# Kernel optimization log

Measured on AMD Instinct MI355X. Metric: run time of the kernel, lower is better.

The kernel has to match this reference:

```python
import jax, jax.numpy as jnp
import numpy as np

B, T, D = 8, 1024, 768
H, DH = 12, 64
E, K, DFF = 16, 2, 3072
EPS = 1e-5


def _ln(x, w, b):
    m = x.mean(-1, keepdims=True)
    v = ((x - m) ** 2).mean(-1, keepdims=True)
    return (x - m) * jax.lax.rsqrt(v + EPS) * w + b


def setup_inputs() -> dict:
    key = jax.random.key(0)
    ks = jax.random.split(key, 12)
    s = 0.02
    return {
        "x": jax.random.normal(ks[0], (B, T, D), jnp.float32),
        "ln1_w": jnp.ones((D,), jnp.float32),
        "ln1_b": jnp.zeros((D,), jnp.float32),
        "qkv_w": jax.random.normal(ks[1], (D, 3 * D), jnp.float32) * s,
        "qkv_b": jnp.zeros((3 * D,), jnp.float32),
        "proj_w": jax.random.normal(ks[2], (D, D), jnp.float32) * s,
        "proj_b": jnp.zeros((D,), jnp.float32),
        "ln2_w": jnp.ones((D,), jnp.float32),
        "ln2_b": jnp.zeros((D,), jnp.float32),
        "router_w": jax.random.normal(ks[3], (D, E), jnp.float32) * s,
        "w1": jax.random.normal(ks[4], (E, D, DFF), jnp.float32) * s,
        "b1": jnp.zeros((E, DFF), jnp.float32),
        "w2": jax.random.normal(ks[5], (E, DFF, D), jnp.float32) * s,
        "b2": jnp.zeros((E, D), jnp.float32),
    }


def _block(x, ln1_w, ln1_b, qkv_w, qkv_b, proj_w, proj_b,
           ln2_w, ln2_b, router_w, w1, b1, w2, b2):
    # --- attention ---
    h = _ln(x, ln1_w, ln1_b)
    qkv = h @ qkv_w + qkv_b                      # [B,T,3D]
    q, k, v = jnp.split(qkv, 3, axis=-1)
    q = q.reshape(B, T, H, DH).transpose(0, 2, 1, 3)
    k = k.reshape(B, T, H, DH).transpose(0, 2, 1, 3)
    v = v.reshape(B, T, H, DH).transpose(0, 2, 1, 3)
    scores = jnp.einsum("bhqd,bhkd->bhqk", q, k) / np.sqrt(DH)
    causal = jnp.tril(jnp.ones((T, T), bool))
    scores = jnp.where(causal, scores, -jnp.inf)
    attn = jax.nn.softmax(scores, axis=-1)
    y = jnp.einsum("bhqk,bhkd->bhqd", attn, v)
    y = y.transpose(0, 2, 1, 3).reshape(B, T, D)
    x = x + y @ proj_w + proj_b                  # residual 1

    # --- MoE FFN (dense all-experts, gated combine) ---
    z = _ln(x, ln2_w, ln2_b)                     # [B,T,D]
    probs = jax.nn.softmax(z @ router_w, axis=-1)  # [B,T,E]
    top_p, ix = jax.lax.top_k(probs, K)
    gate = (jax.nn.one_hot(ix, E, dtype=probs.dtype) * top_p[..., None]).sum(-2)  # [B,T,E]
    gate_e = jnp.moveaxis(gate, -1, 0)           # [E,B,T]

    def body(acc, ew):
        g, W1, B1, W2, B2 = ew
        out = jax.nn.gelu(z @ W1 + B1, approximate=False) @ W2 + B2
        return acc + g[..., None] * out, None

    yff, _ = jax.lax.scan(body, jnp.zeros_like(z), (gate_e, w1, b1, w2, b2))
    # MoELayer returns z + yff; Block adds x again (faithful double residual)
    return x + z + yff


def reference(x, ln1_w, ln1_b, qkv_w, qkv_b, proj_w, proj_b,
              ln2_w, ln2_b, router_w, w1, b1, w2, b2):
    return _block(x, ln1_w, ln1_b, qkv_w, qkv_b, proj_w, proj_b,
                  ln2_w, ln2_b, router_w, w1, b1, w2, b2)
```

## Files before the change

### kernel.cpp

```cpp
#include <hip/hip_runtime.h>
#include <math.h>

#define D_MODEL 768
#define T_SEQ   1024
#define B_BATCH 8
#define NTOK    8192
#define H_HEADS 12
#define DHEAD   64
#define NEXP    16
#define DFF     3072
#define NPAIR   16384
#define MAXT128 144
#define MAXT256 80

typedef unsigned short u16;
typedef unsigned int   u32;

typedef __attribute__((ext_vector_type(8))) short bf16x8;
typedef __attribute__((ext_vector_type(4))) float f32x4;
typedef __attribute__((ext_vector_type(4))) u32   u32x4;

__device__ __forceinline__ float bf2f(u16 u) { return __uint_as_float(((u32)u) << 16); }
__device__ __forceinline__ u16 f2bf(float f) {
    u32 u = __float_as_uint(f);
    return (u16)((u + 0x7FFFu + ((u >> 16) & 1u)) >> 16);
}

__device__ __forceinline__ float fast_gelu(float v) {
    float u2 = -1.5957691216f * v * (1.0f + 0.044715f * v * v);
    return v / (1.0f + __expf(u2));
}

__device__ __forceinline__ void gload16(const void* g, void* l) {
    __builtin_amdgcn_global_load_lds((const __attribute__((address_space(1))) void*)g,
                                     (__attribute__((address_space(3))) void*)l, 16, 0, 0);
}

__global__ __launch_bounds__(256) void ln_kernel(const float* __restrict__ x,
                                                 const float* __restrict__ w,
                                                 const float* __restrict__ b,
                                                 u16* __restrict__ out_bf,
                                                 float* __restrict__ out_f) {
    const int row = blockIdx.x;
    const int tid = threadIdx.x;
    const float* xr = x + (size_t)row * D_MODEL;
    float v0 = xr[tid], v1 = xr[tid + 256], v2 = xr[tid + 512];
    float s = v0 + v1 + v2;
    float s2 = v0 * v0 + v1 * v1 + v2 * v2;
#pragma unroll
    for (int o = 32; o > 0; o >>= 1) { s += __shfl_down(s, o); s2 += __shfl_down(s2, o); }
    __shared__ float red[8];
    __shared__ float stats[2];
    const int wid = tid >> 6;
    if ((tid & 63) == 0) { red[wid] = s; red[4 + wid] = s2; }
    __syncthreads();
    if (tid == 0) {
        float ts = red[0] + red[1] + red[2] + red[3];
        float ts2 = red[4] + red[5] + red[6] + red[7];
        float mean = ts * (1.0f / D_MODEL);
        float var = ts2 * (1.0f / D_MODEL) - mean * mean;
        stats[0] = mean;
        stats[1] = rsqrtf(var + 1e-5f);
    }
    __syncthreads();
    const float mean = stats[0], rstd = stats[1];
    u16* orow = out_bf + (size_t)row * D_MODEL;
    float r0 = (v0 - mean) * rstd * w[tid]       + b[tid];
    float r1 = (v1 - mean) * rstd * w[tid + 256] + b[tid + 256];
    float r2 = (v2 - mean) * rstd * w[tid + 512] + b[tid + 512];
    orow[tid] = f2bf(r0); orow[tid + 256] = f2bf(r1); orow[tid + 512] = f2bf(r2);
    if (out_f) {
        float* frow = out_f + (size_t)row * D_MODEL;
        frow[tid] = r0; frow[tid + 256] = r1; frow[tid + 512] = r2;
    }
}

__global__ __launch_bounds__(256) void transpose_cvt(const float* __restrict__ src,
                                                     u16* __restrict__ dst,
                                                     int R, int C) {
    const size_t plane = (size_t)R * C;
    src += (size_t)blockIdx.z * plane;
    dst += (size_t)blockIdx.z * plane;
    __shared__ __align__(16) u16 tile[64][72];
    const int t = threadIdx.x;
    const int r0 = blockIdx.y * 64, c0 = blockIdx.x * 64;
    {
        const int lr = t >> 2, lc = (t & 3) * 16;
        const float* sp = src + (size_t)(r0 + lr) * C + c0 + lc;
        u16 tmp[16];
#pragma unroll
        for (int j = 0; j < 4; ++j) {
            f32x4 f = *(const f32x4*)(sp + j * 4);
            tmp[j * 4 + 0] = f2bf(f[0]); tmp[j * 4 + 1] = f2bf(f[1]);
            tmp[j * 4 + 2] = f2bf(f[2]); tmp[j * 4 + 3] = f2bf(f[3]);
        }
        *(u32x4*)&tile[lr][lc]     = *(const u32x4*)&tmp[0];
        *(u32x4*)&tile[lr][lc + 8] = *(const u32x4*)&tmp[8];
    }
    __syncthreads();
    {
        const int ln = t >> 2, lk0 = (t & 3) * 16;
        u16 o[16];
#pragma unroll
        for (int j = 0; j < 16; ++j) o[j] = tile[lk0 + j][ln];
        u16* d = dst + (size_t)(c0 + ln) * R + r0 + lk0;
        *(u32x4*)&d[0] = *(const u32x4*)&o[0];
        *(u32x4*)&d[8] = *(const u32x4*)&o[8];
    }
}

template <int MODE>
__global__ __launch_bounds__(512, 4) void gemm256(
    const u16* __restrict__ A, const u16* __restrict__ Bt,
    const float* __restrict__ bias, void* __restrict__ Cout,
    const float* __restrict__ resid,
    const int* __restrict__ bucket_tok, const int* __restrict__ offsets,
    const int* __restrict__ counts, const int* __restrict__ desc_e,
    const int* __restrict__ desc_r, const int* __restrict__ tile_cnt,
    int K, int N)
{
    const u32 nwg  = gridDim.x * gridDim.y;
    const u32 orig = blockIdx.x + gridDim.x * blockIdx.y;
    const u32 flat = (nwg & 7u) ? orig : ((orig & 7u) * (nwg >> 3) + (orig >> 3));
    const int bx = (int)(flat % gridDim.x);
    const int by = (int)(flat / gridDim.x);

    int e = 0, r0 = 0, off = 0, ne = 0, row0 = 0;
    const int col0 = bx * 128;
    if constexpr (MODE >= 2) {
        if (by >= *tile_cnt) return;
        e = desc_e[by];
        r0 = desc_r[by];
        off = offsets[e];
        ne = counts[e];
    } else {
        row0 = by * 256;
    }
    if constexpr (MODE == 2) Bt += (size_t)e * D_MODEL * DFF;
    if constexpr (MODE == 3) Bt += (size_t)e * DFF * D_MODEL;

    __shared__ __align__(16) u16 AsBs[256 * 64 + 128 * 64];
    u16* As = AsBs;
    u16* Bs = AsBs + 256 * 64;

    const int tid = threadIdx.x;
    const int lane = tid & 63;
    const int w = tid >> 6;
    const int wm = w >> 1, wn = w & 1;
    const int fr = lane & 15, fg = lane >> 4;

    const int koff = ((((tid & 7) * 16) ^ (((tid >> 3) & 7) << 4)) >> 1);

    u32 aoff[4];
#pragma unroll
    for (int i = 0; i < 4; ++i) {
        const int r = i * 64 + (tid >> 3);
        u32 row;
        if constexpr (MODE == 2) {
            int rb = r0 + r;
            row = (u32)bucket_tok[off + (rb < ne ? rb : 0)];
        } else if constexpr (MODE == 3) {
            int rb = r0 + r;
            row = (u32)(off + (rb < ne ? rb : (ne - 1)));
        } else {
            row = (u32)(row0 + r);
        }
        aoff[i] = row * (u32)K + (u32)koff;
    }
    u32 boff[2];
#pragma unroll
    for (int i = 0; i < 2; ++i) {
        const int n = i * 64 + (tid >> 3);
        boff[i] = (u32)(col0 + n) * (u32)K + (u32)koff;
    }

    f32x4 acc[4][4] = {};

    for (int k0 = 0; k0 < K; k0 += 64) {
        __syncthreads();
#pragma unroll
        for (int i = 0; i < 4; ++i)
            gload16(A + aoff[i] + k0, &As[(i * 512 + w * 64) * 8]);
#pragma unroll
        for (int i = 0; i < 2; ++i)
            gload16(Bt + boff[i] + k0, &Bs[(i * 512 + w * 64) * 8]);
        __syncthreads();
#pragma unroll
        for (int kk = 0; kk < 2; ++kk) {
            const int sw = ((kk * 64 + fg * 16) ^ ((fr & 7) << 4)) >> 1;
            bf16x8 a[4], b[4];
#pragma unroll
            for (int mi = 0; mi < 4; ++mi)
                a[mi] = *(const bf16x8*)&As[(wm * 64 + mi * 16 + fr) * 64 + sw];
#pragma unroll
            for (int ni = 0; ni < 4; ++ni)
                b[ni] = *(const bf16x8*)&Bs[(wn * 64 + ni * 16 + fr) * 64 + sw];
#pragma unroll
            for (int mi = 0; mi < 4; ++mi)
#pragma unroll
                for (int ni = 0; ni < 4; ++ni)
                    acc[mi][ni] = __builtin_amdgcn_mfma_f32_16x16x32_bf16(a[mi], b[ni], acc[mi][ni], 0, 0, 0);
        }
    }

    __syncthreads();
    float* slab = (float*)AsBs + w * 1088;
    const int er = lane >> 2;
    const int ec = (lane & 3) * 16;
    const int colb = col0 + wn * 64 + ec;

#pragma unroll
    for (int mi = 0; mi < 4; ++mi) {
#pragma unroll
        for (int ni = 0; ni < 4; ++ni)
#pragma unroll
            for (int i = 0; i < 4; ++i)
                slab[(fg * 4 + i) * 68 + ni * 16 + fr] = acc[mi][ni][i];
        __syncthreads();
        f32x4 v[4];
#pragma unroll
        for (int q = 0; q < 4; ++q) v[q] = *(const f32x4*)&slab[er * 68 + ec + q * 4];
        const int lrow = wm * 64 + mi * 16 + er;

        if constexpr (MODE == 0) {
            u16 o[16];
#pragma unroll
            for (int q = 0; q < 4; ++q) {
                f32x4 b4 = *(const f32x4*)&bias[colb + q * 4];
#pragma unroll
                for (int j = 0; j < 4; ++j) o[q * 4 + j] = f2bf(v[q][j] + b4[j]);
            }
            u16* cp = (u16*)Cout + (size_t)(row0 + lrow) * N + colb;
            *(u32x4*)cp       = *(const u32x4*)&o[0];
            *(u32x4*)(cp + 8) = *(const u32x4*)&o[8];
        } else if constexpr (MODE == 1) {
            float* cp = (float*)Cout + (size_t)(row0 + lrow) * N + colb;
            const float* rp = resid + (size_t)(row0 + lrow) * N + colb;
#pragma unroll
            for (int q = 0; q < 4; ++q) {
                f32x4 b4 = *(const f32x4*)&bias[colb + q * 4];
                f32x4 r4 = *(const f32x4*)(rp + q * 4);
                f32x4 o4;
#pragma unroll
                for (int j = 0; j < 4; ++j) o4[j] = v[q][j] + b4[j] + r4[j];
                *(f32x4*)(cp + q * 4) = o4;
            }
        } else if constexpr (MODE == 2) {
            const int rb = r0 + lrow;
            if (rb < ne) {
                u16 o[16];
#pragma unroll
                for (int q = 0; q < 4; ++q) {
                    f32x4 b4 = *(const f32x4*)&bias[(size_t)e * DFF + colb + q * 4];
#pragma unroll
                    for (int j = 0; j < 4; ++j) o[q * 4 + j] = f2bf(fast_gelu(v[q][j] + b4[j]));
                }
                u16* cp = (u16*)Cout + (size_t)(off + rb) * N + colb;
                *(u32x4*)cp       = *(const u32x4*)&o[0];
                *(u32x4*)(cp + 8) = *(const u32x4*)&o[8];
            }
        } else {
            const int rb = r0 + lrow;
            if (rb < ne) {
                float* cp = (float*)Cout + (size_t)(off + rb) * N + colb;
#pragma unroll
                for (int q = 0; q < 4; ++q) {
                    f32x4 b4 = *(const f32x4*)&bias[(size_t)e * D_MODEL + colb + q * 4];
                    f32x4 o4;
#pragma unroll
                    for (int j = 0; j < 4; ++j) o4[j] = v[q][j] + b4[j];
                    *(f32x4*)(cp + q * 4) = o4;
                }
            }
        }
        if (mi < 3) __syncthreads();
    }
}

template <int MODE>
__global__ __launch_bounds__(256) void gemm128f(
    const u16* __restrict__ A, const float* __restrict__ Bf,
    const float* __restrict__ bias, void* __restrict__ Cout,
    const float* __restrict__ resid,
    const int* __restrict__ bucket_tok, const int* __restrict__ offsets,
    const int* __restrict__ counts, const int* __restrict__ desc_e,
    const int* __restrict__ desc_r, const int* __restrict__ tile_cnt,
    int K, int N)
{
    int e = 0, r0 = 0, off = 0, ne = 0, row0 = 0;
    const int col0 = blockIdx.x * 128;
    if constexpr (MODE >= 2) {
        if ((int)blockIdx.y >= *tile_cnt) return;
        e = desc_e[blockIdx.y]; r0 = desc_r[blockIdx.y];
        off = offsets[e]; ne = counts[e];
    } else row0 = blockIdx.y * 128;
    if constexpr (MODE == 2) Bf += (size_t)e * D_MODEL * DFF;
    if constexpr (MODE == 3) Bf += (size_t)e * DFF * D_MODEL;

    __shared__ __align__(16) u16 AsL[128 * 32];
    __shared__ __align__(16) u16 BsL[128 * 32];

    const int tid = threadIdx.x;
    const int lane = tid & 63;
    const int w = tid >> 6;
    const int wr = (w >> 1) * 64, wc = (w & 1) * 64;
    const int fr = lane & 15, fg = lane >> 4;
    const int lrow = lane >> 2, lk = (lane & 3) * 8;

    const u16* ag[2];
#pragma unroll
    for (int i = 0; i < 2; ++i) {
        int r = i * 64 + w * 16 + lrow;
        size_t srow;
        if constexpr (MODE == 2) {
            int rb = r0 + r;
            int tok = bucket_tok[off + (rb < ne ? rb : 0)];
            srow = (size_t)tok * K;
        } else if constexpr (MODE == 3) {
            int rb = r0 + r;
            int pp = off + (rb < ne ? rb : (ne - 1));
            srow = (size_t)pp * K;
        } else srow = (size_t)(row0 + r) * K;
        ag[i] = A + srow + lk;
    }

    f32x4 acc[4][4] = {};
    for (int k0 = 0; k0 < K; k0 += 32) {
        __syncthreads();
        gload16(ag[0] + k0, &AsL[0 * 2048 + w * 512]);
        gload16(ag[1] + k0, &AsL[1 * 2048 + w * 512]);
#pragma unroll
        for (int i = 0; i < 4; ++i) {
            int s = tid + 256 * i;
            int kk = s >> 5, n4 = (s & 31) * 4;
            f32x4 f = *(const f32x4*)(Bf + (size_t)(k0 + kk) * N + col0 + n4);
            BsL[(n4 + 0) * 32 + kk] = f2bf(f[0]);
            BsL[(n4 + 1) * 32 + kk] = f2bf(f[1]);
            BsL[(n4 + 2) * 32 + kk] = f2bf(f[2]);
            BsL[(n4 + 3) * 32 + kk] = f2bf(f[3]);
        }
        __syncthreads();
        bf16x8 a[4], b[4];
#pragma unroll
        for (int mi = 0; mi < 4; ++mi)
            a[mi] = *(const bf16x8*)&AsL[(wr + mi * 16 + fr) * 32 + fg * 8];
#pragma unroll
        for (int ni = 0; ni < 4; ++ni)
            b[ni] = *(const bf16x8*)&BsL[(wc + ni * 16 + fr) * 32 + fg * 8];
#pragma unroll
        for (int mi = 0; mi < 4; ++mi)
#pragma unroll
            for (int ni = 0; ni < 4; ++ni)
                acc[mi][ni] = __builtin_amdgcn_mfma_f32_16x16x32_bf16(a[mi], b[ni], acc[mi][ni], 0, 0, 0);
    }
#pragma unroll
    for (int mi = 0; mi < 4; ++mi) {
#pragma unroll
        for (int ni = 0; ni < 4; ++ni) {
            const int lr = wr + mi * 16 + fg * 4;
            const int col = col0 + wc + ni * 16 + fr;
#pragma unroll
            for (int i = 0; i < 4; ++i) {
                float v = acc[mi][ni][i];
                if constexpr (MODE == 0) {
                    int grow = row0 + lr + i;
                    ((u16*)Cout)[(size_t)grow * N + col] = f2bf(v + bias[col]);
                } else if constexpr (MODE == 1) {
                    int grow = row0 + lr + i;
                    size_t idx = (size_t)grow * N + col;
                    ((float*)Cout)[idx] = resid[idx] + v + bias[col];
                } else if constexpr (MODE == 2) {
                    int rb = r0 + lr + i;
                    if (rb < ne) {
                        float vb = v + bias[(size_t)e * DFF + col];
                        ((u16*)Cout)[(size_t)(off + rb) * N + col] = f2bf(fast_gelu(vb));
                    }
                } else {
                    int rb = r0 + lr + i;
                    if (rb < ne) {
                        ((float*)Cout)[(size_t)(off + rb) * N + col] = v + bias[(size_t)e * D_MODEL + col];
                    }
                }
            }
        }
    }
}

__global__ __launch_bounds__(256) void attn_mfma(const u16* __restrict__ qkv,
                                                 u16* __restrict__ y) {
    const int bh = blockIdx.x;
    const int b = bh / H_HEADS, h = bh % H_HEADS;
    const int qt = gridDim.y - 1 - blockIdx.y;
    const int tid = threadIdx.x, lane = tid & 63, w = tid >> 6;
    const int fr = lane & 15, fg = lane >> 4;

    __shared__ __align__(16) u16 Ks[64][72];
    __shared__ __align__(16) u16 Vt[64][72];
    __shared__ __align__(16) u16 Ps[4][32][72];

    const int tb = b * T_SEQ + qt * 128;
    const int wrow = w * 32;

    bf16x8 aq[2][2];
#pragma unroll
    for (int rg = 0; rg < 2; ++rg) {
        const u16* qp = qkv + (size_t)(tb + wrow + rg * 16 + fr) * (3 * D_MODEL) + h * DHEAD + fg * 8;
        aq[rg][0] = *(const bf16x8*)qp;
        aq[rg][1] = *(const bf16x8*)(qp + 32);
    }
    f32x4 accO[2][4] = {};
    float m_[2][4], l_[2][4];
#pragma unroll
    for (int rg = 0; rg < 2; ++rg)
#pragma unroll
        for (int i = 0; i < 4; ++i) { m_[rg][i] = -1e30f; l_[rg][i] = 0.0f; }

    const int ktmax = 2 * qt + 1;
    for (int kt = 0; kt <= ktmax; ++kt) {
        __syncthreads();
        {
            const int krow = tid >> 2, c16 = (tid & 3) * 16;
            const u16* kp = qkv + (size_t)(b * T_SEQ + kt * 64 + krow) * (3 * D_MODEL)
                          + D_MODEL + h * DHEAD + c16;
            *(u32x4*)&Ks[krow][c16]     = *(const u32x4*)kp;
            *(u32x4*)&Ks[krow][c16 + 8] = *(const u32x4*)(kp + 8);
            const u16* vp = kp + D_MODEL;
            u16 vv[16];
            *(u32x4*)&vv[0] = *(const u32x4*)vp;
            *(u32x4*)&vv[8] = *(const u32x4*)(vp + 8);
#pragma unroll
            for (int j = 0; j < 16; ++j) Vt[c16 + j][krow] = vv[j];
        }
        __syncthreads();

        if (kt * 64 > qt * 128 + wrow + 31) continue;

#pragma unroll
        for (int rg = 0; rg < 2; ++rg) {
            f32x4 s4[4] = {};
#pragma unroll
            for (int kk = 0; kk < 2; ++kk) {
#pragma unroll
                for (int ni = 0; ni < 4; ++ni) {
                    bf16x8 bk = *(const bf16x8*)&Ks[ni * 16 + fr][kk * 32 + fg * 8];
                    s4[ni] = __builtin_amdgcn_mfma_f32_16x16x32_bf16(aq[rg][kk], bk, s4[ni], 0, 0, 0);
                }
            }
            float p[4][4];
#pragma unroll
            for (int i = 0; i < 4; ++i) {
                const int grow = qt * 128 + wrow + rg * 16 + fg * 4 + i;
                float rmax = -1e30f;
#pragma unroll
                for (int ni = 0; ni < 4; ++ni) {
                    float v = s4[ni][i] * 0.125f;
                    if (kt * 64 + ni * 16 + fr > grow) v = -1e30f;
                    p[ni][i] = v;
                    rmax = fmaxf(rmax, v);
                }
#pragma unroll
                for (int msk = 1; msk < 16; msk <<= 1) rmax = fmaxf(rmax, __shfl_xor(rmax, msk));
                const float mn = fmaxf(m_[rg][i], rmax);
                float sum = 0.0f;
#pragma unroll
                for (int ni = 0; ni < 4; ++ni) {
                    float ev = __expf(p[ni][i] - mn);
                    p[ni][i] = ev;
                    sum += ev;
                }
#pragma unroll
                for (int msk = 1; msk < 16; msk <<= 1) sum += __shfl_xor(sum, msk);
                const float sc = __expf(m_[rg][i] - mn);
                l_[rg][i] = l_[rg][i] * sc + sum;
                m_[rg][i] = mn;
#pragma unroll
                for (int ni = 0; ni < 4; ++ni) accO[rg][ni][i] *= sc;
#pragma unroll
                for (int ni = 0; ni < 4; ++ni)
                    Ps[w][rg * 16 + fg * 4 + i][ni * 16 + fr] = f2bf(p[ni][i]);
            }
        }

#pragma unroll
        for (int rg = 0; rg < 2; ++rg) {
#pragma unroll
            for (int kk = 0; kk < 2; ++kk) {
                bf16x8 ap = *(const bf16x8*)&Ps[w][rg * 16 + fr][kk * 32 + fg * 8];
#pragma unroll
                for (int ni = 0; ni < 4; ++ni) {
                    bf16x8 bv = *(const bf16x8*)&Vt[ni * 16 + fr][kk * 32 + fg * 8];
                    accO[rg][ni] = __builtin_amdgcn_mfma_f32_16x16x32_bf16(ap, bv, accO[rg][ni], 0, 0, 0);
                }
            }
        }
    }

#pragma unroll
    for (int rg = 0; rg < 2; ++rg) {
#pragma unroll
        for (int i = 0; i < 4; ++i) {
            const float inv = 1.0f / l_[rg][i];
            u16* yp = y + (size_t)(tb + wrow + rg * 16 + fg * 4 + i) * D_MODEL + h * DHEAD;
#pragma unroll
            for (int ni = 0; ni < 4; ++ni) yp[ni * 16 + fr] = f2bf(accO[rg][ni][i] * inv);
        }
    }
}

__global__ __launch_bounds__(64) void router_kernel(const float* __restrict__ z,
                                                    const float* __restrict__ rw,
                                                    float* __restrict__ gates,
                                                    int* __restrict__ eidx) {
    const int t = blockIdx.x;
    const int lane = threadIdx.x;
    const int e = lane & 15, part = lane >> 4;
    const float* zr = z + (size_t)t * D_MODEL;
    float acc = 0.0f;
    for (int d = part * 192; d < part * 192 + 192; ++d)
        acc += zr[d] * rw[d * NEXP + e];
    acc += __shfl_down(acc, 32);
    acc += __shfl_down(acc, 16);
    const float lg = acc;
    float logit[NEXP];
#pragma unroll
    for (int ee = 0; ee < NEXP; ++ee) logit[ee] = __shfl(lg, ee);
    if (lane == 0) {
        float m1 = -1e30f, m2 = -1e30f; int i1 = 0, i2 = 0;
#pragma unroll
        for (int ee = 0; ee < NEXP; ++ee) {
            float v = logit[ee];
            if (v > m1) { m2 = m1; i2 = i1; m1 = v; i1 = ee; }
            else if (v > m2) { m2 = v; i2 = ee; }
        }
        float den = 0.0f;
#pragma unroll
        for (int ee = 0; ee < NEXP; ++ee) den += __expf(logit[ee] - m1);
        const float inv = 1.0f / den;
        gates[2 * t] = inv;
        gates[2 * t + 1] = __expf(m2 - m1) * inv;
        eidx[2 * t] = i1;
        eidx[2 * t + 1] = i2;
    }
}

__global__ __launch_bounds__(256) void count_kernel(const int* __restrict__ eidx, int* counts) {
    int i = blockIdx.x * 256 + threadIdx.x;
    if (i < NPAIR) atomicAdd(&counts[eidx[i]], 1);
}

__global__ void offsets_kernel(const int* __restrict__ counts, int* offsets, int* cursor,
                               int* desc_e, int* desc_r, int* tile_cnt, int step) {
    if (threadIdx.x == 0 && blockIdx.x == 0) {
        int off = 0, nt = 0;
        for (int e = 0; e < NEXP; ++e) {
            offsets[e] = off;
            cursor[e] = off;
            int c = counts[e];
            for (int r = 0; r < c; r += step) { desc_e[nt] = e; desc_r[nt] = r; ++nt; }
            off += c;
        }
        *tile_cnt = nt;
    }
}

__global__ __launch_bounds__(256) void scatter_kernel(const int* __restrict__ eidx, int* cursor,
                                                      int* __restrict__ btok, int* __restrict__ ppos) {
    int i = blockIdx.x * 256 + threadIdx.x;
    if (i < NPAIR) {
        int pos = atomicAdd(&cursor[eidx[i]], 1);
        btok[pos] = i >> 1;
        ppos[i] = pos;
    }
}

__global__ __launch_bounds__(256) void final_kernel(const float* __restrict__ x1,
                                                    const float* __restrict__ zf,
                                                    const float* __restrict__ moe_o,
                                                    const float* __restrict__ gates,
                                                    const int* __restrict__ ppos,
                                                    float* __restrict__ out) {
    const int t = blockIdx.x;
    const int d = blockIdx.y * 256 + threadIdx.x;
    const size_t idx = (size_t)t * D_MODEL + d;
    const float g0 = gates[2 * t], g1 = gates[2 * t + 1];
    const int p0 = ppos[2 * t], p1 = ppos[2 * t + 1];
    out[idx] = x1[idx] + zf[idx] + g0 * moe_o[(size_t)p0 * D_MODEL + d]
                                 + g1 * moe_o[(size_t)p1 * D_MODEL + d];
}

extern "C" void kernel_launch(void* const* d_in, const int* in_sizes, int n_in,
                              void* d_out, int out_size, void* d_ws, size_t ws_size,
                              hipStream_t stream) {
    const float* x        = (const float*)d_in[0];
    const float* ln1_w    = (const float*)d_in[1];
    const float* ln1_b    = (const float*)d_in[2];
    const float* qkv_w    = (const float*)d_in[3];
    const float* qkv_b    = (const float*)d_in[4];
    const float* proj_w   = (const float*)d_in[5];
    const float* proj_b   = (const float*)d_in[6];
    const float* ln2_w    = (const float*)d_in[7];
    const float* ln2_b    = (const float*)d_in[8];
    const float* router_w = (const float*)d_in[9];
    const float* w1       = (const float*)d_in[10];
    const float* b1       = (const float*)d_in[11];
    const float* w2       = (const float*)d_in[12];
    const float* b2       = (const float*)d_in[13];
    float* out = (float*)d_out;

    char* ws = (char*)d_ws;
    size_t off = 0;
    auto alloc = [&](size_t bytes) -> void* {
        void* p = ws + off;
        off += (bytes + 255) & ~(size_t)255;
        return p;
    };
    u16*  h_bf   = (u16*)alloc((size_t)NTOK * D_MODEL * 2);
    u16*  qkv_bf = (u16*)alloc((size_t)NTOK * 3 * D_MODEL * 2);
    u16*  y_bf   = h_bf;
    float* x1    = (float*)alloc((size_t)NTOK * D_MODEL * 4);
    u16*  z_bf   = (u16*)alloc((size_t)NTOK * D_MODEL * 2);
    float* z_f   = (float*)alloc((size_t)NTOK * D_MODEL * 4);
    u16*  act    = (u16*)alloc((size_t)NPAIR * DFF * 2);
    float* moe_o = (float*)alloc((size_t)NPAIR * D_MODEL * 4);
    float* gates = (float*)alloc((size_t)NTOK * 2 * 4);
    int*  eidx   = (int*)alloc((size_t)NTOK * 2 * 4);
    int*  ppos   = (int*)alloc((size_t)NTOK * 2 * 4);
    int*  btok   = (int*)alloc((size_t)NPAIR * 4);
    int*  counts = (int*)alloc(NEXP * 4);
    int*  offs   = (int*)alloc(NEXP * 4);
    int*  cursor = (int*)alloc(NEXP * 4);
    int*  desc_e = (int*)alloc(MAXT128 * 4);
    int*  desc_r = (int*)alloc(MAXT128 * 4);
    int*  tcnt   = (int*)alloc(4);
    u16* qkvT  = (u16*)alloc((size_t)(3 * D_MODEL) * D_MODEL * 2);
    u16* projT = (u16*)alloc((size_t)D_MODEL * D_MODEL * 2);
    u16* w1t   = (u16*)alloc((size_t)NEXP * DFF * D_MODEL * 2);
    u16* w2t   = (u16*)alloc((size_t)NEXP * D_MODEL * DFF * 2);
    const bool useT = (off <= ws_size);
    (void)in_sizes; (void)n_in; (void)out_size;

    hipMemsetAsync(counts, 0, NEXP * 4, stream);

    if (useT) {
        transpose_cvt<<<dim3(3 * D_MODEL / 64, D_MODEL / 64, 1), 256, 0, stream>>>(qkv_w, qkvT, D_MODEL, 3 * D_MODEL);
        transpose_cvt<<<dim3(D_MODEL / 64, D_MODEL / 64, 1), 256, 0, stream>>>(proj_w, projT, D_MODEL, D_MODEL);
        transpose_cvt<<<dim3(DFF / 64, D_MODEL / 64, NEXP), 256, 0, stream>>>(w1, w1t, D_MODEL, DFF);
        transpose_cvt<<<dim3(D_MODEL / 64, DFF / 64, NEXP), 256, 0, stream>>>(w2, w2t, DFF, D_MODEL);
    }

    ln_kernel<<<NTOK, 256, 0, stream>>>(x, ln1_w, ln1_b, h_bf, nullptr);
    if (useT)
        gemm256<0><<<dim3(18, 32), 512, 0, stream>>>(h_bf, qkvT, qkv_b, qkv_bf, nullptr,
            nullptr, nullptr, nullptr, nullptr, nullptr, nullptr, D_MODEL, 3 * D_MODEL);
    else
        gemm128f<0><<<dim3(18, 64), 256, 0, stream>>>(h_bf, qkv_w, qkv_b, qkv_bf, nullptr,
            nullptr, nullptr, nullptr, nullptr, nullptr, nullptr, D_MODEL, 3 * D_MODEL);

    attn_mfma<<<dim3(B_BATCH * H_HEADS, T_SEQ / 128), 256, 0, stream>>>(qkv_bf, y_bf);

    if (useT)
        gemm256<1><<<dim3(6, 32), 512, 0, stream>>>(y_bf, projT, proj_b, x1, x,
            nullptr, nullptr, nullptr, nullptr, nullptr, nullptr, D_MODEL, D_MODEL);
    else
        gemm128f<1><<<dim3(6, 64), 256, 0, stream>>>(y_bf, proj_w, proj_b, x1, x,
            nullptr, nullptr, nullptr, nullptr, nullptr, nullptr, D_MODEL, D_MODEL);

    ln_kernel<<<NTOK, 256, 0, stream>>>(x1, ln2_w, ln2_b, z_bf, z_f);
    router_kernel<<<NTOK, 64, 0, stream>>>(z_f, router_w, gates, eidx);
    count_kernel<<<NPAIR / 256, 256, 0, stream>>>(eidx, counts);
    offsets_kernel<<<1, 64, 0, stream>>>(counts, offs, cursor, desc_e, desc_r, tcnt,
                                         useT ? 256 : 128);
    scatter_kernel<<<NPAIR / 256, 256, 0, stream>>>(eidx, cursor, btok, ppos);

    if (useT) {
        gemm256<2><<<dim3(DFF / 128, MAXT256), 512, 0, stream>>>(z_bf, w1t, b1, act, nullptr,
            btok, offs, counts, desc_e, desc_r, tcnt, D_MODEL, DFF);
        gemm256<3><<<dim3(D_MODEL / 128, MAXT256), 512, 0, stream>>>(act, w2t, b2, moe_o, nullptr,
            btok, offs, counts, desc_e, desc_r, tcnt, DFF, D_MODEL);
    } else {
        gemm128f<2><<<dim3(DFF / 128, MAXT128), 256, 0, stream>>>(z_bf, w1, b1, act, nullptr,
            btok, offs, counts, desc_e, desc_r, tcnt, D_MODEL, DFF);
        gemm128f<3><<<dim3(D_MODEL / 128, MAXT128), 256, 0, stream>>>(act, w2, b2, moe_o, nullptr,
            btok, offs, counts, desc_e, desc_r, tcnt, DFF, D_MODEL);
    }

    final_kernel<<<dim3(NTOK, 3), 256, 0, stream>>>(x1, z_f, moe_o, gates, ppos, out);
}
```

Before: 665.2 us.

## Double-buffer GEMM LDS, fold Q scale into QKV epilogue, tune attention and final kernels

The 256x128 GEMM now double-buffers its A/B tiles in LDS. Each iteration issues the global loads for tile t+2 while MFMAs run on tile t, using explicit vmcnt waits, raw barriers and setprio, and launch bounds are relaxed to 2 waves per SIMD. The QKV epilogue multiplies the Q columns by 1/sqrt(dh), so attention skips that scale, skips the causal mask on fully unmasked tiles, and rescales the running accumulators only when the max grows. The final combine kernel is vectorised to float4 with one block per token. Together these aim to hide global-load latency and cut ALU and launch work, at the cost of doubled LDS use and lower occupancy.

```diff
diff --git a/kernel.cpp b/kernel.cpp
--- a/kernel.cpp
+++ b/kernel.cpp
@@ -110,7 +110,7 @@
 }
 
 template <int MODE>
-__global__ __launch_bounds__(512, 4) void gemm256(
+__global__ __launch_bounds__(512, 2) void gemmRP(
     const u16* __restrict__ A, const u16* __restrict__ Bt,
     const float* __restrict__ bias, void* __restrict__ Cout,
     const float* __restrict__ resid,
@@ -139,9 +139,8 @@
     if constexpr (MODE == 2) Bt += (size_t)e * D_MODEL * DFF;
     if constexpr (MODE == 3) Bt += (size_t)e * DFF * D_MODEL;
 
-    __shared__ __align__(16) u16 AsBs[256 * 64 + 128 * 64];
-    u16* As = AsBs;
-    u16* Bs = AsBs + 256 * 64;
+    __shared__ __align__(16) u16 As[2][256 * 64];
+    __shared__ __align__(16) u16 Bs[2][128 * 64];
 
     const int tid = threadIdx.x;
     const int lane = tid & 63;
@@ -151,7 +150,7 @@
 
     const int koff = ((((tid & 7) * 16) ^ (((tid >> 3) & 7) << 4)) >> 1);
 
-    u32 aoff[4];
+    u32 aoff[4], boff[2];
 #pragma unroll
     for (int i = 0; i < 4; ++i) {
         const int r = i * 64 + (tid >> 3);
@@ -167,44 +166,76 @@
         }
         aoff[i] = row * (u32)K + (u32)koff;
     }
-    u32 boff[2];
 #pragma unroll
     for (int i = 0; i < 2; ++i) {
         const int n = i * 64 + (tid >> 3);
         boff[i] = (u32)(col0 + n) * (u32)K + (u32)koff;
     }
 
+    auto stage = [&](int buf, int k0) {
+#pragma unroll
+        for (int i = 0; i < 4; ++i)
+            gload16(A + aoff[i] + k0, &As[buf][(i * 512 + w * 64) * 8]);
+#pragma unroll
+        for (int i = 0; i < 2; ++i)
+            gload16(Bt + boff[i] + k0, &Bs[buf][(i * 512 + w * 64) * 8]);
+    };
+
     f32x4 acc[4][4] = {};
-
-    for (int k0 = 0; k0 < K; k0 += 64) {
-        __syncthreads();
-#pragma unroll
-        for (int i = 0; i < 4; ++i)
-            gload16(A + aoff[i] + k0, &As[(i * 512 + w * 64) * 8]);
-#pragma unroll
-        for (int i = 0; i < 2; ++i)
-            gload16(Bt + boff[i] + k0, &Bs[(i * 512 + w * 64) * 8]);
-        __syncthreads();
+    const int nt = K >> 6;
+
+    stage(0, 0);
+    stage(1, 64);
+    asm volatile("s_waitcnt vmcnt(6)" ::: "memory");
+    __builtin_amdgcn_s_barrier();
+
+    for (int t = 0; t < nt; ++t) {
+        const u16* Ac = As[t & 1];
+        const u16* Bc = Bs[t & 1];
+        bf16x8 a[4][2], b[2][2];
 #pragma unroll
         for (int kk = 0; kk < 2; ++kk) {
             const int sw = ((kk * 64 + fg * 16) ^ ((fr & 7) << 4)) >> 1;
-            bf16x8 a[4], b[4];
 #pragma unroll
             for (int mi = 0; mi < 4; ++mi)
-                a[mi] = *(const bf16x8*)&As[(wm * 64 + mi * 16 + fr) * 64 + sw];
-#pragma unroll
-            for (int ni = 0; ni < 4; ++ni)
-                b[ni] = *(const bf16x8*)&Bs[(wn * 64 + ni * 16 + fr) * 64 + sw];
-#pragma unroll
-            for (int mi = 0; mi < 4; ++mi)
-#pragma unroll
-                for (int ni = 0; ni < 4; ++ni)
-                    acc[mi][ni] = __builtin_amdgcn_mfma_f32_16x16x32_bf16(a[mi], b[ni], acc[mi][ni], 0, 0, 0);
+                a[mi][kk] = *(const bf16x8*)&Ac[(wm * 64 + mi * 16 + fr) * 64 + sw];
+#pragma unroll
+            for (int ni = 0; ni < 2; ++ni)
+                b[ni][kk] = *(const bf16x8*)&Bc[(wn * 64 + ni * 16 + fr) * 64 + sw];
+        }
+        bf16x8 b2[2][2];
+#pragma unroll
+        for (int kk = 0; kk < 2; ++kk) {
+            const int sw = ((kk * 64 + fg * 16) ^ ((fr & 7) << 4)) >> 1;
+#pragma unroll
+            for (int ni = 0; ni < 2; ++ni)
+                b2[ni][kk] = *(const bf16x8*)&Bc[(wn * 64 + (ni + 2) * 16 + fr) * 64 + sw];
+        }
+        asm volatile("s_waitcnt lgkmcnt(0)" ::: "memory");
+        __builtin_amdgcn_sched_barrier(0);
+        __builtin_amdgcn_s_barrier();
+        if (t + 2 < nt) stage(t & 1, (t + 2) * 64);
+        __builtin_amdgcn_s_setprio(1);
+#pragma unroll
+        for (int kk = 0; kk < 2; ++kk) {
+#pragma unroll
+            for (int mi = 0; mi < 4; ++mi) {
+                acc[mi][0] = __builtin_amdgcn_mfma_f32_16x16x32_bf16(a[mi][kk], b[0][kk],  acc[mi][0], 0, 0, 0);
+                acc[mi][1] = __builtin_amdgcn_mfma_f32_16x16x32_bf16(a[mi][kk], b[1][kk],  acc[mi][1], 0, 0, 0);
+                acc[mi][2] = __builtin_amdgcn_mfma_f32_16x16x32_bf16(a[mi][kk], b2[0][kk], acc[mi][2], 0, 0, 0);
+                acc[mi][3] = __builtin_amdgcn_mfma_f32_16x16x32_bf16(a[mi][kk], b2[1][kk], acc[mi][3], 0, 0, 0);
+            }
+        }
+        __builtin_amdgcn_s_setprio(0);
+        if (t + 1 < nt) {
+            if (t + 2 < nt) asm volatile("s_waitcnt vmcnt(6)" ::: "memory");
+            else            asm volatile("s_waitcnt vmcnt(0)" ::: "memory");
+            __builtin_amdgcn_s_barrier();
         }
     }
 
     __syncthreads();
-    float* slab = (float*)AsBs + w * 1088;
+    float* slab = (float*)&As[0][0] + w * 1088;
     const int er = lane >> 2;
     const int ec = (lane & 3) * 16;
     const int colb = col0 + wn * 64 + ec;
@@ -223,12 +254,13 @@
         const int lrow = wm * 64 + mi * 16 + er;
 
         if constexpr (MODE == 0) {
+            const float qs = (colb < D_MODEL) ? 0.125f : 1.0f;
             u16 o[16];
 #pragma unroll
             for (int q = 0; q < 4; ++q) {
                 f32x4 b4 = *(const f32x4*)&bias[colb + q * 4];
 #pragma unroll
-                for (int j = 0; j < 4; ++j) o[q * 4 + j] = f2bf(v[q][j] + b4[j]);
+                for (int j = 0; j < 4; ++j) o[q * 4 + j] = f2bf((v[q][j] + b4[j]) * qs);
             }
             u16* cp = (u16*)Cout + (size_t)(row0 + lrow) * N + colb;
             *(u32x4*)cp       = *(const u32x4*)&o[0];
@@ -364,7 +396,8 @@
                 float v = acc[mi][ni][i];
                 if constexpr (MODE == 0) {
                     int grow = row0 + lr + i;
-                    ((u16*)Cout)[(size_t)grow * N + col] = f2bf(v + bias[col]);
+                    const float qs = (col < D_MODEL) ? 0.125f : 1.0f;
+                    ((u16*)Cout)[(size_t)grow * N + col] = f2bf((v + bias[col]) * qs);
                 } else if constexpr (MODE == 1) {
                     int grow = row0 + lr + i;
                     size_t idx = (size_t)grow * N + col;
@@ -434,10 +467,12 @@
         __syncthreads();
 
         if (kt * 64 > qt * 128 + wrow + 31) continue;
+        const bool nomask = (kt * 64 + 63) <= (qt * 128 + wrow);
 
 #pragma unroll
         for (int rg = 0; rg < 2; ++rg) {
             f32x4 s4[4] = {};
+            __builtin_amdgcn_s_setprio(1);
 #pragma unroll
             for (int kk = 0; kk < 2; ++kk) {
 #pragma unroll
@@ -446,21 +481,38 @@
                     s4[ni] = __builtin_amdgcn_mfma_f32_16x16x32_bf16(aq[rg][kk], bk, s4[ni], 0, 0, 0);
                 }
             }
+            __builtin_amdgcn_s_setprio(0);
             float p[4][4];
 #pragma unroll
             for (int i = 0; i < 4; ++i) {
-                const int grow = qt * 128 + wrow + rg * 16 + fg * 4 + i;
                 float rmax = -1e30f;
-#pragma unroll
-                for (int ni = 0; ni < 4; ++ni) {
-                    float v = s4[ni][i] * 0.125f;
-                    if (kt * 64 + ni * 16 + fr > grow) v = -1e30f;
-                    p[ni][i] = v;
-                    rmax = fmaxf(rmax, v);
+                if (nomask) {
+#pragma unroll
+                    for (int ni = 0; ni < 4; ++ni) {
+                        p[ni][i] = s4[ni][i];
+                        rmax = fmaxf(rmax, p[ni][i]);
+                    }
+                } else {
+                    const int grow = qt * 128 + wrow + rg * 16 + fg * 4 + i;
+#pragma unroll
+                    for (int ni = 0; ni < 4; ++ni) {
+                        float v = s4[ni][i];
+                        if (kt * 64 + ni * 16 + fr > grow) v = -1e30f;
+                        p[ni][i] = v;
+                        rmax = fmaxf(rmax, v);
+                    }
                 }
 #pragma unroll
                 for (int msk = 1; msk < 16; msk <<= 1) rmax = fmaxf(rmax, __shfl_xor(rmax, msk));
-                const float mn = fmaxf(m_[rg][i], rmax);
+                float mn = m_[rg][i];
+                if (rmax > mn) {
+                    const float sc = __expf(mn - rmax);
+                    l_[rg][i] *= sc;
+#pragma unroll
+                    for (int ni = 0; ni < 4; ++ni) accO[rg][ni][i] *= sc;
+                    mn = rmax;
+                    m_[rg][i] = rmax;
+                }
                 float sum = 0.0f;
 #pragma unroll
                 for (int ni = 0; ni < 4; ++ni) {
@@ -470,17 +522,14 @@
                 }
 #pragma unroll
                 for (int msk = 1; msk < 16; msk <<= 1) sum += __shfl_xor(sum, msk);
-                const float sc = __expf(m_[rg][i] - mn);
-                l_[rg][i] = l_[rg][i] * sc + sum;
-                m_[rg][i] = mn;
-#pragma unroll
-                for (int ni = 0; ni < 4; ++ni) accO[rg][ni][i] *= sc;
+                l_[rg][i] += sum;
 #pragma unroll
                 for (int ni = 0; ni < 4; ++ni)
                     Ps[w][rg * 16 + fg * 4 + i][ni * 16 + fr] = f2bf(p[ni][i]);
             }
         }
 
+        __builtin_amdgcn_s_setprio(1);
 #pragma unroll
         for (int rg = 0; rg < 2; ++rg) {
 #pragma unroll
@@ -493,6 +542,7 @@
                 }
             }
         }
+        __builtin_amdgcn_s_setprio(0);
     }
 
 #pragma unroll
@@ -573,19 +623,25 @@
     }
 }
 
-__global__ __launch_bounds__(256) void final_kernel(const float* __restrict__ x1,
+__global__ __launch_bounds__(192) void final_kernel(const float* __restrict__ x1,
                                                     const float* __restrict__ zf,
                                                     const float* __restrict__ moe_o,
                                                     const float* __restrict__ gates,
                                                     const int* __restrict__ ppos,
                                                     float* __restrict__ out) {
     const int t = blockIdx.x;
-    const int d = blockIdx.y * 256 + threadIdx.x;
-    const size_t idx = (size_t)t * D_MODEL + d;
+    const int d4 = threadIdx.x * 4;
+    const size_t idx = (size_t)t * D_MODEL + d4;
     const float g0 = gates[2 * t], g1 = gates[2 * t + 1];
     const int p0 = ppos[2 * t], p1 = ppos[2 * t + 1];
-    out[idx] = x1[idx] + zf[idx] + g0 * moe_o[(size_t)p0 * D_MODEL + d]
-                                 + g1 * moe_o[(size_t)p1 * D_MODEL + d];
+    f32x4 a = *(const f32x4*)&x1[idx];
+    f32x4 zz = *(const f32x4*)&zf[idx];
+    f32x4 m0 = *(const f32x4*)&moe_o[(size_t)p0 * D_MODEL + d4];
+    f32x4 m1 = *(const f32x4*)&moe_o[(size_t)p1 * D_MODEL + d4];
+    f32x4 o;
+#pragma unroll
+    for (int j = 0; j < 4; ++j) o[j] = a[j] + zz[j] + g0 * m0[j] + g1 * m1[j];
+    *(f32x4*)&out[idx] = o;
 }
 
 extern "C" void kernel_launch(void* const* d_in, const int* in_sizes, int n_in,
@@ -650,7 +706,7 @@
 
     ln_kernel<<<NTOK, 256, 0, stream>>>(x, ln1_w, ln1_b, h_bf, nullptr);
     if (useT)
-        gemm256<0><<<dim3(18, 32), 512, 0, stream>>>(h_bf, qkvT, qkv_b, qkv_bf, nullptr,
+        gemmRP<0><<<dim3(18, 32), 512, 0, stream>>>(h_bf, qkvT, qkv_b, qkv_bf, nullptr,
             nullptr, nullptr, nullptr, nullptr, nullptr, nullptr, D_MODEL, 3 * D_MODEL);
     else
         gemm128f<0><<<dim3(18, 64), 256, 0, stream>>>(h_bf, qkv_w, qkv_b, qkv_bf, nullptr,
@@ -659,7 +715,7 @@
     attn_mfma<<<dim3(B_BATCH * H_HEADS, T_SEQ / 128), 256, 0, stream>>>(qkv_bf, y_bf);
 
     if (useT)
-        gemm256<1><<<dim3(6, 32), 512, 0, stream>>>(y_bf, projT, proj_b, x1, x,
+        gemmRP<1><<<dim3(6, 32), 512, 0, stream>>>(y_bf, projT, proj_b, x1, x,
             nullptr, nullptr, nullptr, nullptr, nullptr, nullptr, D_MODEL, D_MODEL);
     else
         gemm128f<1><<<dim3(6, 64), 256, 0, stream>>>(y_bf, proj_w, proj_b, x1, x,
@@ -673,9 +729,9 @@
     scatter_kernel<<<NPAIR / 256, 256, 0, stream>>>(eidx, cursor, btok, ppos);
 
     if (useT) {
-        gemm256<2><<<dim3(DFF / 128, MAXT256), 512, 0, stream>>>(z_bf, w1t, b1, act, nullptr,
+        gemmRP<2><<<dim3(DFF / 128, MAXT256), 512, 0, stream>>>(z_bf, w1t, b1, act, nullptr,
             btok, offs, counts, desc_e, desc_r, tcnt, D_MODEL, DFF);
-        gemm256<3><<<dim3(D_MODEL / 128, MAXT256), 512, 0, stream>>>(act, w2t, b2, moe_o, nullptr,
+        gemmRP<3><<<dim3(D_MODEL / 128, MAXT256), 512, 0, stream>>>(act, w2t, b2, moe_o, nullptr,
             btok, offs, counts, desc_e, desc_r, tcnt, DFF, D_MODEL);
     } else {
         gemm128f<2><<<dim3(DFF / 128, MAXT128), 256, 0, stream>>>(z_bf, w1, b1, act, nullptr,
@@ -684,5 +740,5 @@
             btok, offs, counts, desc_e, desc_r, tcnt, DFF, D_MODEL);
     }
 
-    final_kernel<<<dim3(NTOK, 3), 256, 0, stream>>>(x1, z_f, moe_o, gates, ppos, out);
-}
+    final_kernel<<<NTOK, 192, 0, stream>>>(x1, z_f, moe_o, gates, ppos, out);
+}
```

After: 743.3 us. 1.12x slower.
